# Performance work log

Hardware: AMD Instinct MI355X
Metric: run time of the kernel (lower is better)

## Reference

```python
import jax, jax.numpy as jnp
import numpy as np

NUM_HEADS = 8

def setup_inputs() -> dict:
    key = jax.random.key(0)
    ks = jax.random.split(key, 5)
    B, L, D = 4, 2048, 512
    return {
        "query": jax.random.normal(ks[0], (B, L, D), jnp.float32),
        "key":   jax.random.normal(ks[1], (B, L, D), jnp.float32),
        "value": jax.random.normal(ks[2], (B, L, D), jnp.float32),
        "w_out": jax.random.normal(ks[3], (D, D), jnp.float32) * (1.0 / np.sqrt(D)),
        "b_out": jnp.zeros((D,), jnp.float32),
    }

def _scatter_rows(base, idx, vals):
    # base: [L, ...], idx: [u], vals: [u, ...]
    return base.at[idx].set(vals)

_scatter_bh = jax.vmap(jax.vmap(_scatter_rows))  # over (B, H)

def reference(query, key, value, w_out, b_out):
    B, L, D = query.shape
    H = NUM_HEADS
    hd = D // H
    scale = 1.0 / np.sqrt(hd)

    def split(x):
        return x.reshape(B, L, H, hd).transpose(0, 2, 1, 3)  # [B,H,L,hd]
    q, k, v = split(query), split(key), split(value)

    # dense scores for sparsity measure
    scores = jnp.einsum('bhld,bhmd->bhlm', q, k) * scale  # [B,H,L,L]
    m1 = jax.scipy.special.logsumexp(scores, axis=-1) - np.log(L).astype(np.float32)
    m2 = scores.mean(axis=-1)
    M_measure = m1 - m2  # [B,H,L]

    u = max(1, int(np.ceil(np.log(L + 1))))
    _, topk_idx = jax.lax.top_k(M_measure, u)  # [B,H,u]

    v_avg = v.mean(axis=2, keepdims=True)  # [B,H,1,hd]
    default_output = jnp.broadcast_to(v_avg, (B, H, L, hd))

    q_active = jnp.take_along_axis(q, topk_idx[..., None], axis=2)  # [B,H,u,hd]
    scores_active = jnp.einsum('bhud,bhmd->bhum', q_active, k) * scale  # [B,H,u,L]
    attn_weights_active = jax.nn.softmax(scores_active, axis=-1)  # dropout p=0
    attn_output_active = jnp.einsum('bhum,bhmd->bhud', attn_weights_active, v)  # [B,H,u,hd]

    attn_output = _scatter_bh(default_output, topk_idx, attn_output_active)  # [B,H,L,hd]
    attn_weights_full = _scatter_bh(
        jnp.zeros((B, H, L, L), scores.dtype), topk_idx, attn_weights_active)

    out = attn_output.transpose(0, 2, 1, 3).reshape(B, L, D)
    out = out @ w_out.T + b_out
    return out, attn_weights_full
```

## Files before the change

kernel.cpp:

```cpp
#include <hip/hip_runtime.h>
#include <hip/hip_bf16.h>

#define BB 4
#define LL 2048
#define DD 512
#define HH 8
#define HD 64
#define UU 8
#define BH (BB*HH)
#define SCALE 0.125f
#define ASCALE 0.18033688011112042f

typedef __attribute__((ext_vector_type(8))) short short8;
typedef __attribute__((ext_vector_type(4))) float f32x4;
typedef unsigned short ushortT;

#define GLDS(gp, lp) __builtin_amdgcn_global_load_lds( \
    (const __attribute__((address_space(1))) void*)(gp), \
    (__attribute__((address_space(3))) void*)(lp), 16, 0, 0)

__device__ __forceinline__ unsigned short bf16_rne(float x) {
    unsigned int u = __float_as_uint(x);
    unsigned int r = u + 0x7FFFu + ((u >> 16) & 1u);
    return (unsigned short)(r >> 16);
}

__global__ __launch_bounds__(256) void prep(const float* __restrict__ Kin,
                                            const float* __restrict__ Vin,
                                            float* __restrict__ vsum_part,
                                            float* __restrict__ ksum_part,
                                            ushortT* __restrict__ KhiG,
                                            int* __restrict__ map) {
    int t = threadIdx.x;
    if (blockIdx.x < 256) {
        int blk = blockIdx.x;
        if (blk < 32) map[blk*256 + t] = 0;
        int bh = blk & 31, chunk = blk >> 5;
        int b = bh / HH, h = bh % HH;
        int d = t & 63; int g = t >> 6;
        const float* kb = Kin + (size_t)b*LL*DD + h*HD + d;
        const float* vb = Vin + (size_t)b*LL*DD + h*HD + d;
        float ak = 0.f, av = 0.f;
        for (int l = chunk*256 + g; l < chunk*256 + 256; l += 4) {
            ak += kb[(size_t)l*DD]; av += vb[(size_t)l*DD];
        }
        __shared__ float sk[4][64], sv[4][64];
        sk[g][d] = ak; sv[g][d] = av;
        __syncthreads();
        if (g == 0) {
            ksum_part[chunk*2048 + bh*64 + d] = sk[0][d]+sk[1][d]+sk[2][d]+sk[3][d];
            vsum_part[chunk*2048 + bh*64 + d] = sv[0][d]+sv[1][d]+sv[2][d]+sv[3][d];
        }
        return;
    }
    int blk = blockIdx.x - 256;
    int bh = blk >> 5, tile = blk & 31;
    int b = bh / HH, h = bh % HH;
    const float* kb = Kin + (size_t)b*LL*DD + h*HD;
    #pragma unroll
    for (int i = 0; i < 4; i++) {
        int f = t + i*256;
        int row = f >> 4, col4 = f & 15;
        float4 kv = *(const float4*)(kb + (size_t)(tile*64 + row)*DD + col4*4);
        float xs[4] = {kv.x, kv.y, kv.z, kv.w};
        unsigned short hb[4];
        #pragma unroll
        for (int j = 0; j < 4; j++) hb[j] = bf16_rne(xs[j]);
        int off = row*64 + (((col4>>1) ^ (row&7))<<3) + (col4&1)*4;
        uint2 uh; uh.x = hb[0] | ((unsigned)hb[1]<<16); uh.y = hb[2] | ((unsigned)hb[3]<<16);
        *(uint2*)&KhiG[(size_t)blk*4096 + off] = uh;
    }
}

__global__ __launch_bounds__(256) void m_mfma(const float* __restrict__ Q,
                                              const ushortT* __restrict__ KhiG,
                                              const float* __restrict__ ksum_part,
                                              float* __restrict__ Mpart,
                                              float* __restrict__ dotA) {
    int qt = blockIdx.x;
    int bh = blockIdx.y; int b = bh / HH, h = bh % HH;
    int ksp = blockIdx.z;
    const int t = threadIdx.x;
    const int lane = t & 63, w = t >> 6;
    const int c = lane & 15, G = lane >> 4;

    __shared__ unsigned short kHi[2][4096];
    __shared__ float ksLds[64];
    __shared__ float sm[128];

    const float* qb = Q + (size_t)b*LL*DD + h*HD;
    const char* khg = (const char*)(KhiG + (size_t)bh*32*4096);

    short8 a_hi[2][2], a_lo[2][2];
    #pragma unroll
    for (int g = 0; g < 2; g++) {
        int qrow = qt*128 + w*32 + g*16 + c;
        const float* qr = qb + (size_t)qrow*DD + G*8;
        #pragma unroll
        for (int dh = 0; dh < 2; dh++) {
            float4 x0 = *(const float4*)(qr + dh*32);
            float4 x1 = *(const float4*)(qr + dh*32 + 4);
            float x[8] = {x0.x,x0.y,x0.z,x0.w, x1.x,x1.y,x1.z,x1.w};
            short8 hi, lo;
            #pragma unroll
            for (int j = 0; j < 8; j++) {
                float xs = x[j] * ASCALE;
                unsigned short hb = bf16_rne(xs);
                float hf = __uint_as_float((unsigned int)hb << 16);
                hi[j] = (short)hb;
                lo[j] = (short)bf16_rne(xs - hf);
            }
            a_hi[g][dh] = hi; a_lo[g][dh] = lo;
        }
    }
    if (ksp == 0 && t < 64) {
        float s = 0.f;
        #pragma unroll
        for (int cc = 0; cc < 8; cc++) s += ksum_part[cc*2048 + bh*64 + t];
        ksLds[t] = s;
    }

    {
        char* dH = (char*)&kHi[0][0];
        unsigned o0 = w*1024, o1 = w*1024 + 4096;
        const char* sH = khg + (size_t)(ksp*8)*8192;
        GLDS(sH + o0 + lane*16, dH + o0);
        GLDS(sH + o1 + lane*16, dH + o1);
    }
    float se[2][4] = {};
    __syncthreads();

    int rend = ksp*8 + 8;
    for (int r = ksp*8; r < rend; r++) {
        int p = r & 1;
        if (r < rend-1) {
            const char* sH = khg + (size_t)(r+1)*8192;
            char* dH = (char*)&kHi[p^1][0];
            unsigned o0 = w*1024, o1 = w*1024 + 4096;
            GLDS(sH + o0 + lane*16, dH + o0);
            GLDS(sH + o1 + lane*16, dH + o1);
        }
        #pragma unroll
        for (int kt = 0; kt < 4; kt++) {
            int rowIn = kt*16 + c;
            int sw = rowIn & 7;
            int base = rowIn*64;
            short8 bh0 = *(const short8*)&kHi[p][base + ((G       ^ sw)<<3)];
            short8 bh1 = *(const short8*)&kHi[p][base + (((G + 4) ^ sw)<<3)];
            #pragma unroll
            for (int g = 0; g < 2; g++) {
                f32x4 acc = {0.f, 0.f, 0.f, 0.f};
                acc = __builtin_amdgcn_mfma_f32_16x16x32_bf16(a_hi[g][0], bh0, acc, 0, 0, 0);
                acc = __builtin_amdgcn_mfma_f32_16x16x32_bf16(a_hi[g][1], bh1, acc, 0, 0, 0);
                acc = __builtin_amdgcn_mfma_f32_16x16x32_bf16(a_lo[g][0], bh0, acc, 0, 0, 0);
                acc = __builtin_amdgcn_mfma_f32_16x16x32_bf16(a_lo[g][1], bh1, acc, 0, 0, 0);
                #pragma unroll
                for (int q4 = 0; q4 < 4; q4++) se[g][q4] += exp2f(acc[q4]);
            }
        }
        __syncthreads();
    }

    #pragma unroll
    for (int g = 0; g < 2; g++)
        #pragma unroll
        for (int q4 = 0; q4 < 4; q4++) {
            float v = se[g][q4];
            v += __shfl_xor(v, 1);
            v += __shfl_xor(v, 2);
            v += __shfl_xor(v, 4);
            v += __shfl_xor(v, 8);
            se[g][q4] = v;
        }
    if (c == 0) {
        #pragma unroll
        for (int g = 0; g < 2; g++)
            #pragma unroll
            for (int q4 = 0; q4 < 4; q4++)
                sm[w*32 + g*16 + G*4 + q4] = se[g][q4];
    }
    __syncthreads();
    if (t < 128) {
        int qrow = qt*128 + t;
        Mpart[((size_t)ksp*BH + bh)*LL + qrow] = sm[t];
        if (ksp == 0) {
            const float* qr = qb + (size_t)qrow*DD;
            float dot = 0.f;
            for (int d0 = 0; d0 < 64; d0 += 4) {
                float4 qv = *(const float4*)(qr + d0);
                dot += qv.x*ksLds[d0] + qv.y*ksLds[d0+1] + qv.z*ksLds[d0+2] + qv.w*ksLds[d0+3];
            }
            dotA[bh*LL + qrow] = dot * (SCALE/(float)LL);
        }
    }
}

__global__ __launch_bounds__(256) void top8_defo(const float* __restrict__ Mpart,
                                                 const float* __restrict__ dotA,
                                                 const float* __restrict__ vsum_part,
                                                 const float* __restrict__ w_out,
                                                 const float* __restrict__ b_out,
                                                 int* __restrict__ map,
                                                 float* __restrict__ defo) {
    int t = threadIdx.x;
    __shared__ float Ml[LL];
    __shared__ float vals[256];
    __shared__ int   vidx[256];
    if (blockIdx.x >= BH) {
        int b = blockIdx.x - BH;
        for (int i = t; i < DD; i += 256) {
            float s = 0.f;
            #pragma unroll
            for (int cc = 0; cc < 8; cc++)
                s += vsum_part[cc*2048 + (b*HH + (i >> 6))*64 + (i & 63)];
            Ml[i] = s * (1.0f/LL);
        }
        __syncthreads();
        for (int dp = t; dp < DD; dp += 256) {
            const float* wr = w_out + (size_t)dp*DD;
            float acc = b_out[dp];
            for (int d0 = 0; d0 < DD; d0 += 4) {
                float4 wv = *(const float4*)(wr + d0);
                acc += Ml[d0]*wv.x + Ml[d0+1]*wv.y + Ml[d0+2]*wv.z + Ml[d0+3]*wv.w;
            }
            defo[b*DD + dp] = acc;
        }
        return;
    }
    int bh = blockIdx.x;
    for (int i = t; i < LL; i += 256) {
        float s = Mpart[(size_t)bh*LL + i]
                + Mpart[((size_t)BH + bh)*LL + i]
                + Mpart[((size_t)2*BH + bh)*LL + i]
                + Mpart[((size_t)3*BH + bh)*LL + i];
        Ml[i] = __logf(s) - __logf((float)LL) - dotA[bh*LL + i];
    }
    __syncthreads();
    for (int r = 0; r < UU; r++) {
        float bv = -1e30f; int bi = 0;
        for (int i = t; i < LL; i += 256) {
            float v = Ml[i];
            if (v > bv) { bv = v; bi = i; }
        }
        vals[t] = bv; vidx[t] = bi;
        __syncthreads();
        for (int s = 128; s > 0; s >>= 1) {
            if (t < s) {
                if (vals[t+s] > vals[t] ||
                    (vals[t+s] == vals[t] && vidx[t+s] < vidx[t])) {
                    vals[t] = vals[t+s]; vidx[t] = vidx[t+s];
                }
            }
            __syncthreads();
        }
        if (t == 0) {
            int w = vidx[0];
            Ml[w] = -1e30f;
            atomicOr(&map[(bh/HH)*LL + w], 1 << (bh % HH));
        }
        __syncthreads();
    }
}

__global__ __launch_bounds__(256) void out_mega(const float* __restrict__ Q,
                                                const float* __restrict__ Kin,
                                                const float* __restrict__ Vin,
                                                const float* __restrict__ defo,
                                                const float* __restrict__ vsum_part,
                                                const int* __restrict__ map,
                                                const float* __restrict__ w_out,
                                                const float* __restrict__ b_out,
                                                float* __restrict__ out,
                                                float* __restrict__ Wfull) {
    int l = blockIdx.x, b = blockIdx.y;
    int t = threadIdx.x;

    {
        int fid = b*LL + l;
        f32x4* Wz = (f32x4*)Wfull;
        const f32x4 z = {0.f, 0.f, 0.f, 0.f};
        #pragma unroll
        for (int rr = 0; rr < 8; rr++) {
            int R = fid*8 + rr;
            int bh2 = R >> 11, l2 = R & 2047;
            int b2 = bh2 >> 3, h2 = bh2 & 7;
            if (!((map[b2*LL + l2] >> h2) & 1)) {
                f32x4* rowp = Wz + (size_t)R*512;
                rowp[t] = z;
                rowp[t + 256] = z;
            }
        }
    }

    float* orow = out + ((size_t)b*LL + l) * DD;
    int mp = map[b*LL + l];
    if (mp == 0) {
        const float* dr = defo + b*DD;
        orow[t] = dr[t]; orow[t + 256] = dr[t + 256];
        return;
    }

    __shared__ float x[DD];
    __shared__ float qs[64];
    __shared__ float w[LL];
    __shared__ float red[256];
    __shared__ float red4[16][16][4];
    for (int i = t; i < DD; i += 256) {
        float s = 0.f;
        #pragma unroll
        for (int cc = 0; cc < 8; cc++)
            s += vsum_part[cc*2048 + (b*HH + (i >> 6))*64 + (i & 63)];
        x[i] = s * (1.0f/LL);
    }
    __syncthreads();

    for (int h = 0; h < HH; h++) if (mp & (1 << h)) {
        int bh = b*HH + h;
        if (t < 64) qs[t] = Q[(size_t)b*LL*DD + (size_t)l*DD + h*HD + t];
        __syncthreads();
        const float* kb = Kin + (size_t)b*LL*DD + h*HD;
        float s[8];
        float mx = -1e30f;
        #pragma unroll
        for (int p = 0; p < 8; p++) {
            int m = t + p*256;
            const float* kr = kb + (size_t)m*DD;
            float acc = 0.f;
            for (int d0 = 0; d0 < 64; d0 += 4) {
                float4 kv = *(const float4*)(kr + d0);
                acc += qs[d0]*kv.x + qs[d0+1]*kv.y + qs[d0+2]*kv.z + qs[d0+3]*kv.w;
            }
            s[p] = acc * SCALE;
            mx = fmaxf(mx, s[p]);
        }
        red[t] = mx; __syncthreads();
        for (int st = 128; st > 0; st >>= 1) { if (t < st) red[t] = fmaxf(red[t], red[t+st]); __syncthreads(); }
        mx = red[0]; __syncthreads();
        float lsum = 0.f;
        #pragma unroll
        for (int p = 0; p < 8; p++) { s[p] = __expf(s[p] - mx); lsum += s[p]; }
        red[t] = lsum; __syncthreads();
        for (int st = 128; st > 0; st >>= 1) { if (t < st) red[t] += red[t+st]; __syncthreads(); }
        float inv = 1.0f / red[0]; __syncthreads();
        float* wrow = Wfull + ((size_t)bh*LL + l) * LL;
        #pragma unroll
        for (int p = 0; p < 8; p++) {
            int m = (p << 8) + t;
            float wn = s[p] * inv;
            w[m] = wn;
            wrow[m] = wn;
        }
        __syncthreads();
        const float4* vb4 = (const float4*)(Vin + (size_t)b*LL*DD + h*HD);
        int grp = t >> 4, d4 = t & 15;
        f32x4 acc4 = {0.f, 0.f, 0.f, 0.f};
        for (int it = 0; it < 128; it++) {
            int m = grp + it*16;
            float4 v4 = vb4[(size_t)m*128 + d4];
            float wm = w[m];
            acc4[0] += wm * v4.x; acc4[1] += wm * v4.y;
            acc4[2] += wm * v4.z; acc4[3] += wm * v4.w;
        }
        *(f32x4*)&red4[grp][d4][0] = acc4;
        __syncthreads();
        if (t < 64) {
            int dq = t >> 2, comp = t & 3;
            float sum = 0.f;
            #pragma unroll
            for (int g = 0; g < 16; g++) sum += red4[g][dq][comp];
            x[h*64 + t] = sum;
        }
        __syncthreads();
    }

    for (int dp = t; dp < DD; dp += 256) {
        const float* wr = w_out + (size_t)dp*DD;
        float acc = b_out[dp];
        for (int d0 = 0; d0 < DD; d0 += 4) {
            float4 wv = *(const float4*)(wr + d0);
            acc += x[d0]*wv.x + x[d0+1]*wv.y + x[d0+2]*wv.z + x[d0+3]*wv.w;
        }
        orow[dp] = acc;
    }
}

extern "C" void kernel_launch(void* const* d_in, const int* in_sizes, int n_in,
                              void* d_out, int out_size, void* d_ws, size_t ws_size,
                              hipStream_t stream) {
    const float* Q     = (const float*)d_in[0];
    const float* Kin   = (const float*)d_in[1];
    const float* Vin   = (const float*)d_in[2];
    const float* w_out = (const float*)d_in[3];
    const float* b_out = (const float*)d_in[4];

    float* out   = (float*)d_out;
    float* Wfull = out + (size_t)BB*LL*DD;

    char* ws = (char*)d_ws;
    float*   vsum_part = (float*)(ws);
    float*   ksum_part = (float*)(ws + 65536);
    float*   Mpart     = (float*)(ws + 131072);
    float*   dotA      = (float*)(ws + 1179648);
    int*     map       = (int*)  (ws + 1441792);
    float*   defo      = (float*)(ws + 1474560);
    ushortT* KhiG      = (ushortT*)(ws + (2u<<20));

    prep<<<1280, 256, 0, stream>>>(Kin, Vin, vsum_part, ksum_part, KhiG, map);
    m_mfma<<<dim3(16, BH, 4), 256, 0, stream>>>(Q, KhiG, ksum_part, Mpart, dotA);
    top8_defo<<<BH + BB, 256, 0, stream>>>(Mpart, dotA, vsum_part, w_out, b_out, map, defo);
    out_mega<<<dim3(LL, BB), 256, 0, stream>>>(Q, Kin, Vin, defo, vsum_part, map,
                                               w_out, b_out, out, Wfull);
}
```

Baseline: 349.1 us.

## Move attention-weight zero-fill into the score kernel as extra blocks

Measured after the change: 366.5 us. 5.0% more time.

```diff
diff --git a/kernel.cpp b/kernel.cpp
--- a/kernel.cpp
+++ b/kernel.cpp
@@ -72,15 +72,26 @@
     }
 }
 
-__global__ __launch_bounds__(256) void m_mfma(const float* __restrict__ Q,
-                                              const ushortT* __restrict__ KhiG,
-                                              const float* __restrict__ ksum_part,
-                                              float* __restrict__ Mpart,
-                                              float* __restrict__ dotA) {
-    int qt = blockIdx.x;
-    int bh = blockIdx.y; int b = bh / HH, h = bh % HH;
-    int ksp = blockIdx.z;
+__global__ __launch_bounds__(256) void m_mfma_fill(const float* __restrict__ Q,
+                                                   const ushortT* __restrict__ KhiG,
+                                                   const float* __restrict__ ksum_part,
+                                                   float* __restrict__ Mpart,
+                                                   float* __restrict__ dotA,
+                                                   f32x4* __restrict__ Wz) {
     const int t = threadIdx.x;
+    int bid = blockIdx.x;
+    if (bid >= 2048) {
+        size_t fid = (size_t)(bid - 2048);
+        const f32x4 z = {0.f, 0.f, 0.f, 0.f};
+        f32x4* rowp = Wz + fid*4096;
+        #pragma unroll
+        for (int i = 0; i < 16; i++)
+            rowp[i*256 + t] = z;
+        return;
+    }
+    int qt = bid & 15;
+    int bh = (bid >> 4) & 31; int b = bh / HH, h = bh % HH;
+    int ksp = bid >> 9;
     const int lane = t & 63, w = t >> 6;
     const int c = lane & 15, G = lane >> 4;
 
@@ -262,35 +273,18 @@
     }
 }
 
-__global__ __launch_bounds__(256) void out_mega(const float* __restrict__ Q,
-                                                const float* __restrict__ Kin,
-                                                const float* __restrict__ Vin,
-                                                const float* __restrict__ defo,
-                                                const float* __restrict__ vsum_part,
-                                                const int* __restrict__ map,
-                                                const float* __restrict__ w_out,
-                                                const float* __restrict__ b_out,
-                                                float* __restrict__ out,
-                                                float* __restrict__ Wfull) {
+__global__ __launch_bounds__(256) void out_act(const float* __restrict__ Q,
+                                               const float* __restrict__ Kin,
+                                               const float* __restrict__ Vin,
+                                               const float* __restrict__ defo,
+                                               const float* __restrict__ vsum_part,
+                                               const int* __restrict__ map,
+                                               const float* __restrict__ w_out,
+                                               const float* __restrict__ b_out,
+                                               float* __restrict__ out,
+                                               float* __restrict__ Wfull) {
     int l = blockIdx.x, b = blockIdx.y;
     int t = threadIdx.x;
-
-    {
-        int fid = b*LL + l;
-        f32x4* Wz = (f32x4*)Wfull;
-        const f32x4 z = {0.f, 0.f, 0.f, 0.f};
-        #pragma unroll
-        for (int rr = 0; rr < 8; rr++) {
-            int R = fid*8 + rr;
-            int bh2 = R >> 11, l2 = R & 2047;
-            int b2 = bh2 >> 3, h2 = bh2 & 7;
-            if (!((map[b2*LL + l2] >> h2) & 1)) {
-                f32x4* rowp = Wz + (size_t)R*512;
-                rowp[t] = z;
-                rowp[t + 256] = z;
-            }
-        }
-    }
 
     float* orow = out + ((size_t)b*LL + l) * DD;
     int mp = map[b*LL + l];
@@ -406,8 +400,9 @@
     ushortT* KhiG      = (ushortT*)(ws + (2u<<20));
 
     prep<<<1280, 256, 0, stream>>>(Kin, Vin, vsum_part, ksum_part, KhiG, map);
-    m_mfma<<<dim3(16, BH, 4), 256, 0, stream>>>(Q, KhiG, ksum_part, Mpart, dotA);
+    m_mfma_fill<<<2048 + 8192, 256, 0, stream>>>(Q, KhiG, ksum_part, Mpart, dotA,
+                                                 (f32x4*)Wfull);
     top8_defo<<<BH + BB, 256, 0, stream>>>(Mpart, dotA, vsum_part, w_out, b_out, map, defo);
-    out_mega<<<dim3(LL, BB), 256, 0, stream>>>(Q, Kin, Vin, defo, vsum_part, map,
-                                               w_out, b_out, out, Wfull);
-}
+    out_act<<<dim3(LL, BB), 256, 0, stream>>>(Q, Kin, Vin, defo, vsum_part, map,
+                                              w_out, b_out, out, Wfull);
+}
```
